# Performance work log

Measured on AMD Instinct MI355X. Metric: run time of the kernel, lower is better.

Reference implementation:

```python
import jax, jax.numpy as jnp
import numpy as np

N_PER, B, D, CIN, COUT = 500000, 2, 192, 64, 64
EPS = 1e-5


def _build_coords_and_nbrs():
    rng = np.random.default_rng(0)
    cells, xs, ys, zs = [], [], [], []
    for b in range(B):
        cell = rng.choice(D ** 3, size=N_PER, replace=False).astype(np.int64)
        cells.append(cell + b * D ** 3)
        xs.append(cell // (D * D))
        ys.append((cell // D) % D)
        zs.append(cell % D)
    lin = np.concatenate(cells)
    x = np.concatenate(xs); y = np.concatenate(ys); z = np.concatenate(zs)
    N = lin.shape[0]
    order = np.argsort(lin)
    slin = lin[order]

    def nbrs(axis_stride, cvals):
        cols = []
        for d in (-1, 0, 1):
            tgt = lin + d * axis_stride
            valid = (cvals + d >= 0) & (cvals + d < D)
            pos = np.searchsorted(slin, tgt)
            pc = np.clip(pos, 0, N - 1)
            found = valid & (slin[pc] == tgt)
            cols.append(np.where(found, order[pc], -1))
        return np.stack(cols, axis=1).astype(np.int32)  # [N,3]

    return nbrs(1, z), nbrs(D, y), nbrs(D * D, x)


def setup_inputs() -> dict:
    key = jax.random.key(0)
    k1, k2, k3, k4 = jax.random.split(key, 4)
    nbr_z, nbr_y, nbr_x = _build_coords_and_nbrs()
    N = B * N_PER
    s = 1.0 / np.sqrt(3.0 * CIN)
    return {
        "feats": jax.random.normal(k1, (N, CIN), jnp.float32),
        "W1": jax.random.normal(k2, (3, CIN, CIN), jnp.float32) * s,
        "W2": jax.random.normal(k3, (3, CIN, CIN), jnp.float32) * s,
        "W3": jax.random.normal(k4, (3, CIN, COUT), jnp.float32) * s,
        "gamma": jnp.ones((COUT,), jnp.float32),
        "beta": jnp.zeros((COUT,), jnp.float32),
        "nbr_z": jnp.asarray(nbr_z),
        "nbr_y": jnp.asarray(nbr_y),
        "nbr_x": jnp.asarray(nbr_x),
    }


def _sparse_conv1d(feats, W, nbr):
    # feats [N,Cin], W [3,Cin,Cout], nbr [N,3] (-1 = missing neighbor)
    mask = (nbr >= 0)
    g = feats[jnp.where(mask, nbr, 0)]              # [N,3,Cin] gather
    g = g * mask[..., None].astype(feats.dtype)     # zero missing taps
    return jnp.einsum('nkc,kcd->nd', g, W)          # GEMM over taps


def reference(feats, W1, W2, W3, gamma, beta, nbr_z, nbr_y, nbr_x):
    h = _sparse_conv1d(feats, W1, nbr_z)   # conv (1,1,3)
    h = _sparse_conv1d(h, W2, nbr_y)       # conv (1,3,1)
    h = _sparse_conv1d(h, W3, nbr_x)       # conv (3,1,1)
    # BatchNorm over the N active points (training-mode batch stats)
    mean = jnp.mean(h, axis=0)
    var = jnp.var(h, axis=0)
    h = (h - mean) * (gamma / jnp.sqrt(var + EPS)) + beta
    return jax.nn.relu(h)
```

## Files before the change

kernel.cpp:

```cpp
#include <hip/hip_runtime.h>
#include <cstdint>
#include <cstddef>


typedef __attribute__((ext_vector_type(4))) float float4v;
typedef __attribute__((ext_vector_type(4))) unsigned int uint4v;
typedef __attribute__((ext_vector_type(8))) __bf16 bf16x8;
typedef __attribute__((ext_vector_type(8))) unsigned short ushort8;

__device__ __forceinline__ unsigned short f2bf_bits(float f) {
    unsigned int u = __builtin_bit_cast(unsigned int, f);
    u += 0x7fffu + ((u >> 16) & 1u);
    return (unsigned short)(u >> 16);
}
__device__ __forceinline__ float bf2f(unsigned short b) {
    unsigned int u = ((unsigned int)b) << 16;
    return __builtin_bit_cast(float, u);
}

__global__ __launch_bounds__(256)
void cvt_kernel(const float* __restrict__ in, unsigned short* __restrict__ out,
                size_t n8)
{
    size_t i = (size_t)blockIdx.x * 256 + threadIdx.x;
    const size_t stride = (size_t)gridDim.x * 256;
    for (; i < n8; i += stride) {
        const float4v* p = reinterpret_cast<const float4v*>(in + i * 8);
        float4v f0 = p[0], f1 = p[1];
        ushort8 u;
#pragma unroll
        for (int j = 0; j < 4; ++j) {
            u[j]     = f2bf_bits(f0[j]);
            u[j + 4] = f2bf_bits(f1[j]);
        }
        *reinterpret_cast<uint4v*>(out + i * 8) = __builtin_bit_cast(uint4v, u);
    }
}

__device__ __forceinline__ void issue_tile(
    uint4v (&A)[6], const char* __restrict__ abase,
    const char* __restrict__ zaddr, int i0, int i2,
    int t, int l15, int quad)
{
    const int qo = quad * 16;
    const char* g0 = (i0 >= 0) ? abase + (((size_t)(unsigned)i0) << 7) : zaddr;
    const char* gs = abase + (((size_t)(unsigned)(t * 16 + l15)) << 7);
    const char* g2 = (i2 >= 0) ? abase + (((size_t)(unsigned)i2) << 7) : zaddr;
    A[0] = *reinterpret_cast<const uint4v*>(g0 + qo);
    A[1] = *reinterpret_cast<const uint4v*>(g0 + qo + 64);
    A[2] = *reinterpret_cast<const uint4v*>(gs + qo);
    A[3] = *reinterpret_cast<const uint4v*>(gs + qo + 64);
    A[4] = *reinterpret_cast<const uint4v*>(g2 + qo);
    A[5] = *reinterpret_cast<const uint4v*>(g2 + qo + 64);
}

template<bool DO_STATS>
__device__ __forceinline__ void conv_tile(
    const uint4v (&A)[6], const unsigned short* __restrict__ Bld,
    unsigned short* __restrict__ tl, unsigned short* __restrict__ Hout,
    int t, int lane, int l15, int quad,
    float (&lsum)[4], float (&lsq)[4])
{
    float4v acc[4] = {};
#pragma unroll
    for (int s = 0; s < 6; ++s) {
        bf16x8 a = __builtin_bit_cast(bf16x8, A[s]);
#pragma unroll
        for (int nt = 0; nt < 4; ++nt) {
            uint4v ub = *reinterpret_cast<const uint4v*>(
                Bld + (((s * 4 + nt) * 64 + lane) << 3));
            bf16x8 b = __builtin_bit_cast(bf16x8, ub);
            acc[nt] = __builtin_amdgcn_mfma_f32_16x16x32_bf16(a, b, acc[nt], 0, 0, 0);
        }
    }
    if (DO_STATS) {
#pragma unroll
        for (int nt = 0; nt < 4; ++nt) {
            lsum[nt] += acc[nt][0] + acc[nt][1] + acc[nt][2] + acc[nt][3];
            lsq[nt]  += acc[nt][0] * acc[nt][0] + acc[nt][1] * acc[nt][1]
                      + acc[nt][2] * acc[nt][2] + acc[nt][3] * acc[nt][3];
        }
    }
#pragma unroll
    for (int nt = 0; nt < 4; ++nt)
#pragma unroll
        for (int r = 0; r < 4; ++r)
            tl[(quad * 4 + r) * 72 + nt * 16 + l15] = f2bf_bits(acc[nt][r]);
    __asm__ volatile("s_waitcnt lgkmcnt(0)" ::: "memory");
    unsigned short* op = Hout + ((size_t)t << 10);
#pragma unroll
    for (int c = 0; c < 2; ++c) {
        int chunk = c * 64 + lane;
        int r = chunk >> 3;
        int off = (chunk & 7) * 8;
        uint4v v = *reinterpret_cast<const uint4v*>(&tl[r * 72 + off]);
        *reinterpret_cast<uint4v*>(op + (r << 6) + off) = v;
    }
    __asm__ volatile("s_waitcnt lgkmcnt(0)" ::: "memory");
}

template<bool DO_STATS>
__global__ __launch_bounds__(256, 4)
void conv_kernel(const unsigned short* __restrict__ Ain,
                 const float* __restrict__ Wg,
                 const int* __restrict__ nbr,
                 unsigned short* __restrict__ Hout,
                 const unsigned short* __restrict__ Zrow,
                 float* __restrict__ stats, int ntiles)
{
    __shared__ unsigned short Bld[24 * 64 * 8];
    __shared__ unsigned short Tld[4][16 * 72];
    __shared__ float ssum[64], ssq[64];

    const int tid = threadIdx.x;
    for (int i = tid; i < 192 * 64; i += 256) {
        int kc = i >> 6, d = i & 63;
        int tap = kc >> 6, c = kc & 63;
        int s  = tap * 2 + (c >> 5);
        int qd = (c >> 3) & 3, j = c & 7;
        int ln = qd * 16 + (d & 15);
        Bld[(((s * 4 + (d >> 4)) * 64 + ln) << 3) + j] = f2bf_bits(Wg[i]);
    }
    if (DO_STATS && tid < 64) { ssum[tid] = 0.f; ssq[tid] = 0.f; }
    __syncthreads();

    const int lane = tid & 63;
    const int wid  = tid >> 6;
    const int l15  = lane & 15;
    const int quad = lane >> 4;
    const char* abase = (const char*)Ain;
    const char* zaddr = (const char*)Zrow;
    unsigned short* tl = Tld[wid];

    float lsum[4] = {0.f, 0.f, 0.f, 0.f};
    float lsq[4]  = {0.f, 0.f, 0.f, 0.f};

    const int S = gridDim.x * 4;
    int t = blockIdx.x * 4 + wid;
    if (t < ntiles) {
        size_t nb = (size_t)(t * 16 + l15) * 3;
        int iA0 = nbr[nb], iA2 = nbr[nb + 2];
        int iB0 = 0, iB2 = 0;
        uint4v Aa[6], Ab[6];
        issue_tile(Aa, abase, zaddr, iA0, iA2, t, l15, quad);
        int tn = t + S;
        if (tn < ntiles) {
            size_t nb1 = (size_t)(tn * 16 + l15) * 3;
            iA0 = nbr[nb1]; iA2 = nbr[nb1 + 2];
        }
        while (true) {
            int t2 = tn + S;
            if (t2 < ntiles) {
                size_t nb2 = (size_t)(t2 * 16 + l15) * 3;
                iB0 = nbr[nb2]; iB2 = nbr[nb2 + 2];
            }
            if (tn < ntiles)
                issue_tile(Ab, abase, zaddr, iA0, iA2, tn, l15, quad);
            conv_tile<DO_STATS>(Aa, Bld, tl, Hout, t, lane, l15, quad, lsum, lsq);
            t = tn; tn = t2;
            if (t >= ntiles) break;

            t2 = tn + S;
            if (t2 < ntiles) {
                size_t nb2 = (size_t)(t2 * 16 + l15) * 3;
                iA0 = nbr[nb2]; iA2 = nbr[nb2 + 2];
            }
            if (tn < ntiles)
                issue_tile(Aa, abase, zaddr, iB0, iB2, tn, l15, quad);
            conv_tile<DO_STATS>(Ab, Bld, tl, Hout, t, lane, l15, quad, lsum, lsq);
            t = tn; tn = t2;
            if (t >= ntiles) break;
        }
    }

    if (DO_STATS) {
#pragma unroll
        for (int nt = 0; nt < 4; ++nt) {
            atomicAdd(&ssum[nt * 16 + l15], lsum[nt]);
            atomicAdd(&ssq[nt * 16 + l15], lsq[nt]);
        }
        __syncthreads();
        if (tid < 64)               atomicAdd(&stats[tid], ssum[tid]);
        else if (tid < 128)         atomicAdd(&stats[tid], ssq[tid - 64]);
    }
}

__global__ __launch_bounds__(256)
void bn_relu_kernel(const unsigned short* __restrict__ H,
                    const float* __restrict__ stats,
                    const float* __restrict__ gamma,
                    const float* __restrict__ beta,
                    float* __restrict__ out, size_t ntot, float invN)
{
    __shared__ float sscale[64], sbias[64];
    const int tid = threadIdx.x;
    if (tid < 64) {
        float mean = stats[tid] * invN;
        float var  = stats[tid + 64] * invN - mean * mean;
        float sc   = gamma[tid] * rsqrtf(var + 1e-5f);
        sscale[tid] = sc;
        sbias[tid]  = beta[tid] - mean * sc;
    }
    __syncthreads();
    size_t i0 = ((size_t)blockIdx.x * 256 + tid) * 8;
    const size_t stride = (size_t)gridDim.x * 2048;
    const int cb = (int)(i0 & 63);
    float sc[8], bs[8];
#pragma unroll
    for (int j = 0; j < 8; ++j) { sc[j] = sscale[cb + j]; bs[j] = sbias[cb + j]; }
    for (size_t i = i0; i < ntot; i += stride) {
        uint4v v = *reinterpret_cast<const uint4v*>(H + i);
        float4v o0, o1;
#pragma unroll
        for (int j = 0; j < 4; ++j) {
            float lo = bf2f((unsigned short)(v[j] & 0xffffu));
            float hi = bf2f((unsigned short)(v[j] >> 16));
            float r0 = fmaxf(lo * sc[2 * j]     + bs[2 * j],     0.f);
            float r1 = fmaxf(hi * sc[2 * j + 1] + bs[2 * j + 1], 0.f);
            if (j < 2) { o0[2 * j] = r0; o0[2 * j + 1] = r1; }
            else       { o1[2 * (j - 2)] = r0; o1[2 * (j - 2) + 1] = r1; }
        }
        *reinterpret_cast<float4v*>(out + i)     = o0;
        *reinterpret_cast<float4v*>(out + i + 4) = o1;
    }
}

extern "C" void kernel_launch(void* const* d_in, const int* in_sizes, int n_in,
                              void* d_out, int out_size, void* d_ws, size_t ws_size,
                              hipStream_t stream)
{
    const float* feats = (const float*)d_in[0];
    const float* W1    = (const float*)d_in[1];
    const float* W2    = (const float*)d_in[2];
    const float* W3    = (const float*)d_in[3];
    const float* gamma = (const float*)d_in[4];
    const float* beta  = (const float*)d_in[5];
    const int* nbr_z   = (const int*)d_in[6];
    const int* nbr_y   = (const int*)d_in[7];
    const int* nbr_x   = (const int*)d_in[8];

    const int N = in_sizes[0] / 64;
    const int ntiles = N / 16;

    char* ws = (char*)d_ws;
    float* stats = (float*)ws;
    unsigned short* zrow = (unsigned short*)(ws + 512);
    unsigned short* a0 = (unsigned short*)(ws + 1024);
    unsigned short* h1 = a0 + (size_t)N * 64;
    unsigned short* h2 = h1 + (size_t)N * 64;
    unsigned short* h3 = a0;

    hipMemsetAsync(ws, 0, 1024, stream);

    dim3 blk(256);
    cvt_kernel<<<dim3(4096), blk, 0, stream>>>(feats, a0, (size_t)N * 8);
    conv_kernel<false><<<dim3(1024), blk, 0, stream>>>(a0, W1, nbr_z, h1, zrow, nullptr, ntiles);
    conv_kernel<false><<<dim3(1024), blk, 0, stream>>>(h1, W2, nbr_y, h2, zrow, nullptr, ntiles);
    conv_kernel<true ><<<dim3(1024), blk, 0, stream>>>(h2, W3, nbr_x, h3, zrow, stats, ntiles);
    bn_relu_kernel<<<dim3(8192), blk, 0, stream>>>(h3, stats, gamma, beta,
                                                   (float*)d_out, (size_t)N * 64,
                                                   1.0f / (float)N);
}
```

Before: 708.9 us.

## Fuse fp32-to-bf16 conversion into first conv and skip empty neighbor taps

Removes the standalone conversion kernel. A new first-conv kernel gathers fp32 feature rows directly and packs them to bf16 in registers before the MFMAs, which avoids writing and re-reading a bf16 copy of the input. All conv kernels now compute a wave-uniform flag with __any that says whether any row in the tile has a -1/+1 neighbor. When no row does, the MFMAs for that tap are skipped. The cost is roughly twice the register footprint for the fp32 prefetch buffers, with occupancy lowered to 3 blocks per CU, plus extra conversion ALU work in conv1.

```diff
diff --git a/kernel.cpp b/kernel.cpp
--- a/kernel.cpp
+++ b/kernel.cpp
@@ -18,29 +18,74 @@
     return __builtin_bit_cast(float, u);
 }
 
-__global__ __launch_bounds__(256)
-void cvt_kernel(const float* __restrict__ in, unsigned short* __restrict__ out,
-                size_t n8)
-{
-    size_t i = (size_t)blockIdx.x * 256 + threadIdx.x;
-    const size_t stride = (size_t)gridDim.x * 256;
-    for (; i < n8; i += stride) {
-        const float4v* p = reinterpret_cast<const float4v*>(in + i * 8);
-        float4v f0 = p[0], f1 = p[1];
-        ushort8 u;
-#pragma unroll
-        for (int j = 0; j < 4; ++j) {
-            u[j]     = f2bf_bits(f0[j]);
-            u[j + 4] = f2bf_bits(f1[j]);
-        }
-        *reinterpret_cast<uint4v*>(out + i * 8) = __builtin_bit_cast(uint4v, u);
-    }
-}
-
-__device__ __forceinline__ void issue_tile(
+__device__ __forceinline__ void stage_W(const float* __restrict__ Wg,
+                                        unsigned short* __restrict__ Bld, int tid)
+{
+    for (int i = tid; i < 192 * 64; i += 256) {
+        int kc = i >> 6, d = i & 63;
+        int tap = kc >> 6, c = kc & 63;
+        int s  = tap * 2 + (c >> 5);
+        int qd = (c >> 3) & 3, j = c & 7;
+        int ln = qd * 16 + (d & 15);
+        Bld[(((s * 4 + (d >> 4)) * 64 + ln) << 3) + j] = f2bf_bits(Wg[i]);
+    }
+}
+
+__device__ __forceinline__ void mfma_tap(const unsigned short* __restrict__ Bld,
+                                         int lane, bf16x8 a0, bf16x8 a1, int s0,
+                                         float4v (&acc)[4])
+{
+#pragma unroll
+    for (int nt = 0; nt < 4; ++nt) {
+        uint4v ub = *reinterpret_cast<const uint4v*>(
+            Bld + (((s0 * 4 + nt) * 64 + lane) << 3));
+        acc[nt] = __builtin_amdgcn_mfma_f32_16x16x32_bf16(
+            a0, __builtin_bit_cast(bf16x8, ub), acc[nt], 0, 0, 0);
+    }
+#pragma unroll
+    for (int nt = 0; nt < 4; ++nt) {
+        uint4v ub = *reinterpret_cast<const uint4v*>(
+            Bld + ((((s0 + 1) * 4 + nt) * 64 + lane) << 3));
+        acc[nt] = __builtin_amdgcn_mfma_f32_16x16x32_bf16(
+            a1, __builtin_bit_cast(bf16x8, ub), acc[nt], 0, 0, 0);
+    }
+}
+
+template<bool DO_STATS>
+__device__ __forceinline__ void tile_epilogue(const float4v (&acc)[4],
+    unsigned short* __restrict__ tl, unsigned short* __restrict__ Hout,
+    int t, int lane, int l15, int quad, float (&lsum)[4], float (&lsq)[4])
+{
+    if (DO_STATS) {
+#pragma unroll
+        for (int nt = 0; nt < 4; ++nt) {
+            lsum[nt] += acc[nt][0] + acc[nt][1] + acc[nt][2] + acc[nt][3];
+            lsq[nt]  += acc[nt][0] * acc[nt][0] + acc[nt][1] * acc[nt][1]
+                      + acc[nt][2] * acc[nt][2] + acc[nt][3] * acc[nt][3];
+        }
+    }
+#pragma unroll
+    for (int nt = 0; nt < 4; ++nt)
+#pragma unroll
+        for (int r = 0; r < 4; ++r)
+            tl[(quad * 4 + r) * 72 + nt * 16 + l15] = f2bf_bits(acc[nt][r]);
+    __asm__ volatile("s_waitcnt lgkmcnt(0)" ::: "memory");
+    unsigned short* op = Hout + ((size_t)t << 10);
+#pragma unroll
+    for (int c = 0; c < 2; ++c) {
+        int chunk = c * 64 + lane;
+        int r = chunk >> 3;
+        int off = (chunk & 7) * 8;
+        uint4v v = *reinterpret_cast<const uint4v*>(&tl[r * 72 + off]);
+        *reinterpret_cast<uint4v*>(op + (r << 6) + off) = v;
+    }
+    __asm__ volatile("s_waitcnt lgkmcnt(0)" ::: "memory");
+}
+
+
+__device__ __forceinline__ void issue_bf16(
     uint4v (&A)[6], const char* __restrict__ abase,
-    const char* __restrict__ zaddr, int i0, int i2,
-    int t, int l15, int quad)
+    const char* __restrict__ zaddr, int i0, int i2, int t, int l15, int quad)
 {
     const int qo = quad * 16;
     const char* g0 = (i0 >= 0) ? abase + (((size_t)(unsigned)i0) << 7) : zaddr;
@@ -55,48 +100,21 @@
 }
 
 template<bool DO_STATS>
-__device__ __forceinline__ void conv_tile(
-    const uint4v (&A)[6], const unsigned short* __restrict__ Bld,
+__device__ __forceinline__ void consume_bf16(
+    const uint4v (&A)[6], int fl, const unsigned short* __restrict__ Bld,
     unsigned short* __restrict__ tl, unsigned short* __restrict__ Hout,
-    int t, int lane, int l15, int quad,
-    float (&lsum)[4], float (&lsq)[4])
+    int t, int lane, int l15, int quad, float (&lsum)[4], float (&lsq)[4])
 {
     float4v acc[4] = {};
-#pragma unroll
-    for (int s = 0; s < 6; ++s) {
-        bf16x8 a = __builtin_bit_cast(bf16x8, A[s]);
-#pragma unroll
-        for (int nt = 0; nt < 4; ++nt) {
-            uint4v ub = *reinterpret_cast<const uint4v*>(
-                Bld + (((s * 4 + nt) * 64 + lane) << 3));
-            bf16x8 b = __builtin_bit_cast(bf16x8, ub);
-            acc[nt] = __builtin_amdgcn_mfma_f32_16x16x32_bf16(a, b, acc[nt], 0, 0, 0);
-        }
-    }
-    if (DO_STATS) {
-#pragma unroll
-        for (int nt = 0; nt < 4; ++nt) {
-            lsum[nt] += acc[nt][0] + acc[nt][1] + acc[nt][2] + acc[nt][3];
-            lsq[nt]  += acc[nt][0] * acc[nt][0] + acc[nt][1] * acc[nt][1]
-                      + acc[nt][2] * acc[nt][2] + acc[nt][3] * acc[nt][3];
-        }
-    }
-#pragma unroll
-    for (int nt = 0; nt < 4; ++nt)
-#pragma unroll
-        for (int r = 0; r < 4; ++r)
-            tl[(quad * 4 + r) * 72 + nt * 16 + l15] = f2bf_bits(acc[nt][r]);
-    __asm__ volatile("s_waitcnt lgkmcnt(0)" ::: "memory");
-    unsigned short* op = Hout + ((size_t)t << 10);
-#pragma unroll
-    for (int c = 0; c < 2; ++c) {
-        int chunk = c * 64 + lane;
-        int r = chunk >> 3;
-        int off = (chunk & 7) * 8;
-        uint4v v = *reinterpret_cast<const uint4v*>(&tl[r * 72 + off]);
-        *reinterpret_cast<uint4v*>(op + (r << 6) + off) = v;
-    }
-    __asm__ volatile("s_waitcnt lgkmcnt(0)" ::: "memory");
+    if (fl & 1)
+        mfma_tap(Bld, lane, __builtin_bit_cast(bf16x8, A[0]),
+                 __builtin_bit_cast(bf16x8, A[1]), 0, acc);
+    mfma_tap(Bld, lane, __builtin_bit_cast(bf16x8, A[2]),
+             __builtin_bit_cast(bf16x8, A[3]), 2, acc);
+    if (fl & 2)
+        mfma_tap(Bld, lane, __builtin_bit_cast(bf16x8, A[4]),
+                 __builtin_bit_cast(bf16x8, A[5]), 4, acc);
+    tile_epilogue<DO_STATS>(acc, tl, Hout, t, lane, l15, quad, lsum, lsq);
 }
 
 template<bool DO_STATS>
@@ -113,14 +131,7 @@
     __shared__ float ssum[64], ssq[64];
 
     const int tid = threadIdx.x;
-    for (int i = tid; i < 192 * 64; i += 256) {
-        int kc = i >> 6, d = i & 63;
-        int tap = kc >> 6, c = kc & 63;
-        int s  = tap * 2 + (c >> 5);
-        int qd = (c >> 3) & 3, j = c & 7;
-        int ln = qd * 16 + (d & 15);
-        Bld[(((s * 4 + (d >> 4)) * 64 + ln) << 3) + j] = f2bf_bits(Wg[i]);
-    }
+    stage_W(Wg, Bld, tid);
     if (DO_STATS && tid < 64) { ssum[tid] = 0.f; ssq[tid] = 0.f; }
     __syncthreads();
 
@@ -138,36 +149,44 @@
     const int S = gridDim.x * 4;
     int t = blockIdx.x * 4 + wid;
     if (t < ntiles) {
-        size_t nb = (size_t)(t * 16 + l15) * 3;
-        int iA0 = nbr[nb], iA2 = nbr[nb + 2];
-        int iB0 = 0, iB2 = 0;
         uint4v Aa[6], Ab[6];
-        issue_tile(Aa, abase, zaddr, iA0, iA2, t, l15, quad);
+        int flA = 0, flB = 0;
+        int iN0 = 0, iN2 = 0;
+        {
+            size_t nb = (size_t)(t * 16 + l15) * 3;
+            int i0 = nbr[nb], i2 = nbr[nb + 2];
+            flA = (__any(i0 >= 0) ? 1 : 0) | (__any(i2 >= 0) ? 2 : 0);
+            issue_bf16(Aa, abase, zaddr, i0, i2, t, l15, quad);
+        }
         int tn = t + S;
         if (tn < ntiles) {
-            size_t nb1 = (size_t)(tn * 16 + l15) * 3;
-            iA0 = nbr[nb1]; iA2 = nbr[nb1 + 2];
+            size_t nb = (size_t)(tn * 16 + l15) * 3;
+            iN0 = nbr[nb]; iN2 = nbr[nb + 2];
         }
         while (true) {
             int t2 = tn + S;
+            if (tn < ntiles) {
+                flB = (__any(iN0 >= 0) ? 1 : 0) | (__any(iN2 >= 0) ? 2 : 0);
+                issue_bf16(Ab, abase, zaddr, iN0, iN2, tn, l15, quad);
+            }
             if (t2 < ntiles) {
-                size_t nb2 = (size_t)(t2 * 16 + l15) * 3;
-                iB0 = nbr[nb2]; iB2 = nbr[nb2 + 2];
-            }
-            if (tn < ntiles)
-                issue_tile(Ab, abase, zaddr, iA0, iA2, tn, l15, quad);
-            conv_tile<DO_STATS>(Aa, Bld, tl, Hout, t, lane, l15, quad, lsum, lsq);
+                size_t nb = (size_t)(t2 * 16 + l15) * 3;
+                iN0 = nbr[nb]; iN2 = nbr[nb + 2];
+            }
+            consume_bf16<DO_STATS>(Aa, flA, Bld, tl, Hout, t, lane, l15, quad, lsum, lsq);
             t = tn; tn = t2;
             if (t >= ntiles) break;
 
             t2 = tn + S;
+            if (tn < ntiles) {
+                flA = (__any(iN0 >= 0) ? 1 : 0) | (__any(iN2 >= 0) ? 2 : 0);
+                issue_bf16(Aa, abase, zaddr, iN0, iN2, tn, l15, quad);
+            }
             if (t2 < ntiles) {
-                size_t nb2 = (size_t)(t2 * 16 + l15) * 3;
-                iA0 = nbr[nb2]; iA2 = nbr[nb2 + 2];
-            }
-            if (tn < ntiles)
-                issue_tile(Aa, abase, zaddr, iB0, iB2, tn, l15, quad);
-            conv_tile<DO_STATS>(Ab, Bld, tl, Hout, t, lane, l15, quad, lsum, lsq);
+                size_t nb = (size_t)(t2 * 16 + l15) * 3;
+                iN0 = nbr[nb]; iN2 = nbr[nb + 2];
+            }
+            consume_bf16<DO_STATS>(Ab, flB, Bld, tl, Hout, t, lane, l15, quad, lsum, lsq);
             t = tn; tn = t2;
             if (t >= ntiles) break;
         }
@@ -184,6 +203,129 @@
         else if (tid < 128)         atomicAdd(&stats[tid], ssq[tid - 64]);
     }
 }
+
+
+__device__ __forceinline__ void issue_f32(
+    uint4v (&R)[12], const char* __restrict__ fbase,
+    const char* __restrict__ zaddr, int i0, int i2, int t, int l15, int quad)
+{
+    const int qo = quad * 32;
+    const char* g0 = (i0 >= 0) ? fbase + ((size_t)(unsigned)i0) * 256 : zaddr;
+    const char* gs = fbase + ((size_t)(unsigned)(t * 16 + l15)) * 256;
+    const char* g2 = (i2 >= 0) ? fbase + ((size_t)(unsigned)i2) * 256 : zaddr;
+    R[0]  = *reinterpret_cast<const uint4v*>(g0 + qo);
+    R[1]  = *reinterpret_cast<const uint4v*>(g0 + qo + 16);
+    R[2]  = *reinterpret_cast<const uint4v*>(g0 + qo + 128);
+    R[3]  = *reinterpret_cast<const uint4v*>(g0 + qo + 144);
+    R[4]  = *reinterpret_cast<const uint4v*>(gs + qo);
+    R[5]  = *reinterpret_cast<const uint4v*>(gs + qo + 16);
+    R[6]  = *reinterpret_cast<const uint4v*>(gs + qo + 128);
+    R[7]  = *reinterpret_cast<const uint4v*>(gs + qo + 144);
+    R[8]  = *reinterpret_cast<const uint4v*>(g2 + qo);
+    R[9]  = *reinterpret_cast<const uint4v*>(g2 + qo + 16);
+    R[10] = *reinterpret_cast<const uint4v*>(g2 + qo + 128);
+    R[11] = *reinterpret_cast<const uint4v*>(g2 + qo + 144);
+}
+
+__device__ __forceinline__ bf16x8 pack_frag(uint4v lo, uint4v hi)
+{
+    float4v f0 = __builtin_bit_cast(float4v, lo);
+    float4v f1 = __builtin_bit_cast(float4v, hi);
+    ushort8 u;
+#pragma unroll
+    for (int j = 0; j < 4; ++j) {
+        u[j]     = f2bf_bits(f0[j]);
+        u[j + 4] = f2bf_bits(f1[j]);
+    }
+    return __builtin_bit_cast(bf16x8, u);
+}
+
+__device__ __forceinline__ void consume_f32(
+    const uint4v (&R)[12], int fl, const unsigned short* __restrict__ Bld,
+    unsigned short* __restrict__ tl, unsigned short* __restrict__ Hout,
+    int t, int lane, int l15, int quad, float (&lsum)[4], float (&lsq)[4])
+{
+    float4v acc[4] = {};
+    if (fl & 1)
+        mfma_tap(Bld, lane, pack_frag(R[0], R[1]), pack_frag(R[2], R[3]), 0, acc);
+    mfma_tap(Bld, lane, pack_frag(R[4], R[5]), pack_frag(R[6], R[7]), 2, acc);
+    if (fl & 2)
+        mfma_tap(Bld, lane, pack_frag(R[8], R[9]), pack_frag(R[10], R[11]), 4, acc);
+    tile_epilogue<false>(acc, tl, Hout, t, lane, l15, quad, lsum, lsq);
+}
+
+__global__ __launch_bounds__(256, 3)
+void conv1_kernel(const float* __restrict__ Fin,
+                  const float* __restrict__ Wg,
+                  const int* __restrict__ nbr,
+                  unsigned short* __restrict__ Hout,
+                  const float* __restrict__ Zrowf, int ntiles)
+{
+    __shared__ unsigned short Bld[24 * 64 * 8];
+    __shared__ unsigned short Tld[4][16 * 72];
+
+    const int tid = threadIdx.x;
+    stage_W(Wg, Bld, tid);
+    __syncthreads();
+
+    const int lane = tid & 63;
+    const int wid  = tid >> 6;
+    const int l15  = lane & 15;
+    const int quad = lane >> 4;
+    const char* fbase = (const char*)Fin;
+    const char* zaddr = (const char*)Zrowf;
+    unsigned short* tl = Tld[wid];
+
+    float lsum[4] = {0.f, 0.f, 0.f, 0.f};
+    float lsq[4]  = {0.f, 0.f, 0.f, 0.f};
+
+    const int S = gridDim.x * 4;
+    int t = blockIdx.x * 4 + wid;
+    if (t < ntiles) {
+        uint4v Ra[12], Rb[12];
+        int flA = 0, flB = 0;
+        int iN0 = 0, iN2 = 0;
+        {
+            size_t nb = (size_t)(t * 16 + l15) * 3;
+            int i0 = nbr[nb], i2 = nbr[nb + 2];
+            flA = (__any(i0 >= 0) ? 1 : 0) | (__any(i2 >= 0) ? 2 : 0);
+            issue_f32(Ra, fbase, zaddr, i0, i2, t, l15, quad);
+        }
+        int tn = t + S;
+        if (tn < ntiles) {
+            size_t nb = (size_t)(tn * 16 + l15) * 3;
+            iN0 = nbr[nb]; iN2 = nbr[nb + 2];
+        }
+        while (true) {
+            int t2 = tn + S;
+            if (tn < ntiles) {
+                flB = (__any(iN0 >= 0) ? 1 : 0) | (__any(iN2 >= 0) ? 2 : 0);
+                issue_f32(Rb, fbase, zaddr, iN0, iN2, tn, l15, quad);
+            }
+            if (t2 < ntiles) {
+                size_t nb = (size_t)(t2 * 16 + l15) * 3;
+                iN0 = nbr[nb]; iN2 = nbr[nb + 2];
+            }
+            consume_f32(Ra, flA, Bld, tl, Hout, t, lane, l15, quad, lsum, lsq);
+            t = tn; tn = t2;
+            if (t >= ntiles) break;
+
+            t2 = tn + S;
+            if (tn < ntiles) {
+                flA = (__any(iN0 >= 0) ? 1 : 0) | (__any(iN2 >= 0) ? 2 : 0);
+                issue_f32(Ra, fbase, zaddr, iN0, iN2, tn, l15, quad);
+            }
+            if (t2 < ntiles) {
+                size_t nb = (size_t)(t2 * 16 + l15) * 3;
+                iN0 = nbr[nb]; iN2 = nbr[nb + 2];
+            }
+            consume_f32(Rb, flB, Bld, tl, Hout, t, lane, l15, quad, lsum, lsq);
+            t = tn; tn = t2;
+            if (t >= ntiles) break;
+        }
+    }
+}
+
 
 __global__ __launch_bounds__(256)
 void bn_relu_kernel(const unsigned short* __restrict__ H,
@@ -244,17 +386,16 @@
 
     char* ws = (char*)d_ws;
     float* stats = (float*)ws;
+    float* zrowf = (float*)(ws + 512);
     unsigned short* zrow = (unsigned short*)(ws + 512);
-    unsigned short* a0 = (unsigned short*)(ws + 1024);
-    unsigned short* h1 = a0 + (size_t)N * 64;
+    unsigned short* h1 = (unsigned short*)(ws + 1024);
     unsigned short* h2 = h1 + (size_t)N * 64;
-    unsigned short* h3 = a0;
+    unsigned short* h3 = h2 + (size_t)N * 64;
 
     hipMemsetAsync(ws, 0, 1024, stream);
 
     dim3 blk(256);
-    cvt_kernel<<<dim3(4096), blk, 0, stream>>>(feats, a0, (size_t)N * 8);
-    conv_kernel<false><<<dim3(1024), blk, 0, stream>>>(a0, W1, nbr_z, h1, zrow, nullptr, ntiles);
+    conv1_kernel<<<dim3(1024), blk, 0, stream>>>(feats, W1, nbr_z, h1, zrowf, ntiles);
     conv_kernel<false><<<dim3(1024), blk, 0, stream>>>(h1, W2, nbr_y, h2, zrow, nullptr, ntiles);
     conv_kernel<true ><<<dim3(1024), blk, 0, stream>>>(h2, W3, nbr_x, h3, zrow, stats, ntiles);
     bn_relu_kernel<<<dim3(8192), blk, 0, stream>>>(h3, stats, gamma, beta,
```

After: 677.3 us. 4.5% less time.
